# Optimization experiments

Hardware: AMD Instinct MI355X
Metric: run time of the kernel (lower is better)

Reference implementation:

```python
import jax, jax.numpy as jnp
import numpy as np

DIM = 1024
DEPTH = 3
BATCH = 8
SEQ = DIM  # module requires seq_len == dim for the residual add to broadcast


def setup_inputs() -> dict:
    key = jax.random.key(0)
    k1, k2, k3, k4 = jax.random.split(key, 4)
    x = jax.random.normal(k1, (BATCH, SEQ, DIM), dtype=jnp.float32)
    # torch.nn.Linear(dim, 3*dim): weight [3*dim, dim], bias [3*dim]
    Wqkv = jax.random.normal(k2, (3 * DIM, DIM), dtype=jnp.float32) * (1.0 / np.sqrt(DIM))
    bqkv = jax.random.normal(k3, (3 * DIM,), dtype=jnp.float32) * 0.01
    # self.w: Parameter of shape [depth, dim, dim], init randn
    w = jax.random.normal(k4, (DEPTH, DIM, DIM), dtype=jnp.float32)
    return {"x": x, "Wqkv": Wqkv, "bqkv": bqkv, "w": w}


def reference(x, Wqkv, bqkv, w):
    # qkv projection then chunk into q, k, v along last dim
    qkv = x @ Wqkv.T + bqkv                      # [B, S, 3*dim]
    q, k, v = jnp.split(qkv, 3, axis=-1)         # each [B, S, dim]
    scale = 1.0 / (q.shape[-1] ** 0.5)
    # sum over depth of (q @ w[i]) @ k^T, accumulated onto v
    # einsum contracts d (dim), e (dim), and sums over n (depth) in one pass
    scores = jnp.einsum('bsd,nde,bte->bst', q, w, k)  # [B, S, S]; requires S == dim
    return v + scores * scale
```

## Files before the change

kernel.cpp:

```cpp
#include <hip/hip_runtime.h>
#include <hip/hip_bf16.h>
#include <stdint.h>

typedef __bf16 bf16_t;
typedef __bf16 bf16x8 __attribute__((ext_vector_type(8)));
typedef __bf16 bf16x4 __attribute__((ext_vector_type(4)));
typedef float  f32x4  __attribute__((ext_vector_type(4)));

#define DIM   1024
#define BATCH 8
#define NTOK  (BATCH * DIM)
#define SCALE 0.03125f

__global__ void k_cvt(const float* __restrict__ in, bf16_t* __restrict__ out, int n4) {
    int i = blockIdx.x * blockDim.x + threadIdx.x;
    if (i < n4) {
        const float4 v = reinterpret_cast<const float4*>(in)[i];
        bf16x4 o;
        o.x = (bf16_t)v.x; o.y = (bf16_t)v.y; o.z = (bf16_t)v.z; o.w = (bf16_t)v.w;
        reinterpret_cast<bf16x4*>(out)[i] = o;
    }
}

__global__ __launch_bounds__(256)
void k_prep(const float* __restrict__ x, const float* __restrict__ Wqkv,
            const float* __restrict__ w,
            bf16_t* __restrict__ xb, bf16_t* __restrict__ wbig,
            bf16_t* __restrict__ wtb, bf16_t* __restrict__ wqt,
            float* __restrict__ bp32)
{
    __shared__ float tile[32][33];
    const int b = blockIdx.x;
    if (b < 8192) {
        const int i = b * 256 + threadIdx.x;
        const float4 v = reinterpret_cast<const float4*>(x)[i];
        bf16x4 o;
        o.x = (bf16_t)v.x; o.y = (bf16_t)v.y; o.z = (bf16_t)v.z; o.w = (bf16_t)v.w;
        reinterpret_cast<bf16x4*>(xb)[i] = o;
    } else if (b < 10240) {
        const int i = (b - 8192) * 256 + threadIdx.x;
        const float4 v = reinterpret_cast<const float4*>(Wqkv + 1048576)[i];
        bf16x4 o;
        o.x = (bf16_t)v.x; o.y = (bf16_t)v.y; o.z = (bf16_t)v.z; o.w = (bf16_t)v.w;
        reinterpret_cast<bf16x4*>(wbig + 1048576)[i] = o;
    } else if (b < 11264) {
        const int t  = b - 10240;
        const int tx = threadIdx.x & 31, ty = threadIdx.x >> 5;
        const int d0 = (t & 31) * 32, e0 = (t >> 5) * 32;
#pragma unroll
        for (int r = 0; r < 4; ++r) {
            const int d = d0 + r * 8 + ty;
            const int e = e0 + tx;
            tile[r * 8 + ty][tx] =
                w[d * 1024 + e] + w[1048576 + d * 1024 + e] + w[2097152 + d * 1024 + e];
        }
        __syncthreads();
#pragma unroll
        for (int r = 0; r < 4; ++r) {
            const int e = e0 + r * 8 + ty;
            const int d = d0 + tx;
            wtb[e * 1024 + d] = (bf16_t)tile[tx][r * 8 + ty];
        }
    } else if (b < 12288) {
        const int t  = b - 11264;
        const int tx = threadIdx.x & 31, ty = threadIdx.x >> 5;
        const int e0 = (t & 31) * 32, d0 = (t >> 5) * 32;
#pragma unroll
        for (int r = 0; r < 4; ++r)
            tile[r * 8 + ty][tx] = Wqkv[(long)(e0 + r * 8 + ty) * 1024 + d0 + tx];
        __syncthreads();
#pragma unroll
        for (int r = 0; r < 4; ++r)
            wqt[(long)(d0 + r * 8 + ty) * 1024 + e0 + tx] = (bf16_t)tile[tx][r * 8 + ty];
    } else {
        const int i = (b - 12288) * 256 + threadIdx.x;
        const f32x4 z = {0.f, 0.f, 0.f, 0.f};
        reinterpret_cast<f32x4*>(bp32)[i] = z;
    }
}

__global__ __launch_bounds__(256)
void k_mid(const float* __restrict__ bq, const bf16_t* __restrict__ wtb,
           const bf16_t* __restrict__ wqt, float* __restrict__ bqwO,
           float* __restrict__ oAt)
{
    __shared__ __align__(16) bf16_t As[128 * 32];
    __shared__ __align__(16) bf16_t Bs[128 * 32];

    const int tid  = threadIdx.x;
    const int wave = tid >> 6;
    const int lane = tid & 63;

    if (blockIdx.x < 256) {
        const int n = blockIdx.x * 4 + wave;
        const bf16_t* row = wtb + (long)n * 1024;
        float s = 0.f;
#pragma unroll
        for (int c = 0; c < 2; ++c) {
            const int d0 = (lane + c * 64) * 8;
            const bf16x8 v = *reinterpret_cast<const bf16x8*>(row + d0);
#pragma unroll
            for (int e = 0; e < 8; ++e) s += bq[d0 + e] * (float)v[e];
        }
#pragma unroll
        for (int off = 32; off; off >>= 1) s += __shfl_down(s, off);
        if (lane == 0) bqwO[n] = s;
        return;
    }

    const int s  = blockIdx.x - 256;
    const int bm = (s >> 5) * 128;
    const int bn = ((s >> 2) & 7) * 128;
    const int kb = (s & 3) * 256;
    const int wr = wave >> 1, wc = wave & 1;
    const int lhi = lane >> 4, llo = lane & 15;

    f32x4 acc[4][4];
    const f32x4 fz = {0.f, 0.f, 0.f, 0.f};
#pragma unroll
    for (int i = 0; i < 4; ++i)
#pragma unroll
        for (int j = 0; j < 4; ++j) acc[i][j] = fz;

    for (int k0 = 0; k0 < 256; k0 += 32) {
#pragma unroll
        for (int i = 0; i < 2; ++i) {
            const int c  = wave * 128 + i * 64 + lane;
            const int r  = c >> 2;
            const int cc = (c & 3) << 3;
            const long ga = (long)(bm + r) * 1024 + kb + k0 + cc;
            const long gb = (long)(bn + r) * 1024 + kb + k0 + cc;
            const int lbase = (wave * 128 + i * 64) << 3;
            __builtin_amdgcn_global_load_lds(
                (const __attribute__((address_space(1))) uint32_t*)(wtb + ga),
                (__attribute__((address_space(3))) uint32_t*)(&As[lbase]), 16, 0, 0);
            __builtin_amdgcn_global_load_lds(
                (const __attribute__((address_space(1))) uint32_t*)(wqt + gb),
                (__attribute__((address_space(3))) uint32_t*)(&Bs[lbase]), 16, 0, 0);
        }
        __syncthreads();

        bf16x8 af[4], bfr[4];
#pragma unroll
        for (int mi = 0; mi < 4; ++mi)
            af[mi] = *reinterpret_cast<const bf16x8*>(&As[(wr * 64 + mi * 16 + llo) * 32 + lhi * 8]);
#pragma unroll
        for (int ni = 0; ni < 4; ++ni)
            bfr[ni] = *reinterpret_cast<const bf16x8*>(&Bs[(wc * 64 + ni * 16 + llo) * 32 + lhi * 8]);
#pragma unroll
        for (int mi = 0; mi < 4; ++mi)
#pragma unroll
            for (int ni = 0; ni < 4; ++ni)
                acc[mi][ni] = __builtin_amdgcn_mfma_f32_16x16x32_bf16(af[mi], bfr[ni], acc[mi][ni], 0, 0, 0);
        __syncthreads();
    }

#pragma unroll
    for (int mi = 0; mi < 4; ++mi) {
        const int r0 = bm + wr * 64 + mi * 16 + lhi * 4;
#pragma unroll
        for (int ni = 0; ni < 4; ++ni) {
            const int cg = bn + wc * 64 + ni * 16 + llo;
            const f32x4 v = acc[mi][ni];
#pragma unroll
            for (int j = 0; j < 4; ++j)
                atomicAdd(&oAt[(long)(r0 + j) * 1024 + cg], v[j]);
        }
    }
}

template<int BN_, int MODE>
__global__ __launch_bounds__(512, 2)
void k_db(const bf16_t* __restrict__ A, const bf16_t* __restrict__ Bp,
          const float* __restrict__ bqw, const float* __restrict__ bqkv,
          bf16_t* __restrict__ oQW, bf16_t* __restrict__ oK, float* __restrict__ oF)
{
    constexpr int NF   = BN_ / 64;
    constexpr int LB   = BN_ / 64;
    constexpr int LPT  = 2 + LB;
    constexpr int SLOT = (128 + BN_) * 128;
    constexpr int NTT  = 16;
    __shared__ __align__(16) unsigned char slds[2 * SLOT];

    const int tid  = threadIdx.x;
    const int wave = tid >> 6, lane = tid & 63;
    const int wm = wave >> 2, wn = wave & 3;
    const int llo = lane & 15, lhi = lane >> 4;

    int bm, bn; long zz = 0;
    if (MODE == 1) {
        bm = blockIdx.x * 128; bn = blockIdx.y * BN_;
    } else {
        const int nw = ((int)blockIdx.x & 7) * 64 + ((int)blockIdx.x >> 3);
        zz = (long)(nw >> 6) << 20;
        const int r = nw & 63;
        bm = (r >> 3) * 128; bn = (r & 7) * 128;
    }

    const bf16_t* sp[LPT]; int dst[LPT];
#pragma unroll
    for (int j = 0; j < 2; ++j) {
        const int C = j * 512 + tid;
        const int r = C >> 3, u = (C & 7) ^ (r & 7);
        sp[j] = A + zz + (long)(bm + r) * 1024 + (u << 3);
        dst[j] = C << 4;
    }
#pragma unroll
    for (int j = 0; j < LB; ++j) {
        const int C = j * 512 + tid;
        const int r = C >> 3, u = (C & 7) ^ (r & 7);
        sp[2 + j] = Bp + zz + (long)(bn + r) * 1024 + (u << 3);
        dst[2 + j] = 16384 + (C << 4);
    }

    auto stage = [&](int tt) {
        unsigned char* s = &slds[(tt & 1) * SLOT];
        const long ko = (long)tt << 6;
#pragma unroll
        for (int j = 0; j < LPT; ++j)
            __builtin_amdgcn_global_load_lds(
                (const __attribute__((address_space(1))) uint32_t*)(sp[j] + ko),
                (__attribute__((address_space(3))) uint32_t*)(s + dst[j]), 16, 0, 0);
    };

    f32x4 acc[4][NF];
    const f32x4 fz = {0.f, 0.f, 0.f, 0.f};
#pragma unroll
    for (int i = 0; i < 4; ++i)
#pragma unroll
        for (int j = 0; j < NF; ++j) acc[i][j] = fz;

    stage(0);

    for (int t = 0; t < NTT; ++t) {
        if (t + 1 < NTT) {
            stage(t + 1);
            asm volatile("s_waitcnt vmcnt(%0)" :: "i"(LPT) : "memory");
        } else {
            asm volatile("s_waitcnt vmcnt(0)" ::: "memory");
        }
        __builtin_amdgcn_s_barrier();

        const unsigned char* sb = &slds[(t & 1) * SLOT];
#pragma unroll
        for (int ks = 0; ks < 2; ++ks) {
            bf16x8 af[4], bfv[NF];
#pragma unroll
            for (int mi = 0; mi < 4; ++mi) {
                const int r = wm * 64 + mi * 16 + llo;
                af[mi] = *reinterpret_cast<const bf16x8*>(
                    sb + r * 128 + ((((ks << 2) | lhi) ^ (r & 7)) << 4));
            }
#pragma unroll
            for (int ni = 0; ni < NF; ++ni) {
                const int r = wn * (NF * 16) + ni * 16 + llo;
                bfv[ni] = *reinterpret_cast<const bf16x8*>(
                    sb + 16384 + r * 128 + ((((ks << 2) | lhi) ^ (r & 7)) << 4));
            }
            __builtin_amdgcn_s_setprio(1);
#pragma unroll
            for (int mi = 0; mi < 4; ++mi)
#pragma unroll
                for (int ni = 0; ni < NF; ++ni)
                    acc[mi][ni] = __builtin_amdgcn_mfma_f32_16x16x32_bf16(
                        af[mi], bfv[ni], acc[mi][ni], 0, 0, 0);
            __builtin_amdgcn_s_setprio(0);
        }
        asm volatile("s_waitcnt lgkmcnt(0)" ::: "memory");
        __builtin_amdgcn_s_barrier();
    }

#pragma unroll
    for (int mi = 0; mi < 4; ++mi) {
        const long r0 = bm + wm * 64 + mi * 16 + lhi * 4;
#pragma unroll
        for (int ni = 0; ni < NF; ++ni) {
            const int cg = bn + wn * (NF * 16) + ni * 16 + llo;
            const f32x4 v = acc[mi][ni];
            if (MODE == 1) {
                const int sec = cg >> 10;
                const int c1  = cg & 1023;
                const float bb = (sec == 0) ? bqw[cg] : bqkv[cg];
#pragma unroll
                for (int j = 0; j < 4; ++j) {
                    const long idx = (r0 + j) * 1024 + c1;
                    const float val = v[j] + bb;
                    if (sec == 0)      oQW[idx] = (bf16_t)val;
                    else if (sec == 1) oK[idx] = (bf16_t)val;
                    else               oF[idx] = val;
                }
            } else {
#pragma unroll
                for (int j = 0; j < 4; ++j) {
                    const long idx = zz + (r0 + j) * 1024 + cg;
                    oF[idx] = oF[idx] + SCALE * v[j];
                }
            }
        }
    }
}

extern "C" void kernel_launch(void* const* d_in, const int* in_sizes, int n_in,
                              void* d_out, int out_size, void* d_ws, size_t ws_size,
                              hipStream_t stream) {
    const float* x    = (const float*)d_in[0];
    const float* Wqkv = (const float*)d_in[1];
    const float* bqkv = (const float*)d_in[2];
    const float* w    = (const float*)d_in[3];
    float* out = (float*)d_out;

    char* ws = (char*)d_ws;
    bf16_t* xb   = (bf16_t*)(ws);
    bf16_t* wbig = (bf16_t*)(ws + (16l << 20));
    float*  bqw  = (float*) (ws + (22l << 20));
    bf16_t* kb   = (bf16_t*)(ws + (22l << 20) + 65536);
    bf16_t* qwb  = (bf16_t*)(ws + (38l << 20) + 65536);
    bf16_t* wtb  = qwb;
    bf16_t* wqt  = qwb + 1048576;
    float*  bp32 = (float*)(qwb + 2097152);
    if (ws_size < (size_t)(54l << 20) + 65536) return;

    k_prep<<<13312, 256, 0, stream>>>(x, Wqkv, w, xb, wbig, wtb, wqt, bp32);

    k_mid<<<512, 256, 0, stream>>>(bqkv, wtb, wqt, bqw, bp32);

    k_cvt<<<1024, 256, 0, stream>>>(bp32, wbig, 262144);

    k_db<192, 1><<<dim3(64, 16), 512, 0, stream>>>(xb, wbig, bqw, bqkv, qwb, kb, out);

    k_db<128, 2><<<dim3(512), 512, 0, stream>>>(qwb, kb, nullptr, nullptr,
                                                nullptr, nullptr, out);
}
```

Before: 117.0 us.

## Halve k_db K-tile to 32 and raise occupancy to 4 blocks per CU

Shrinks the double-buffered LDS K-tile from 64 to 32 elements and doubles the number of K iterations, using a new swizzle that packs two 32-element rows into each 128-byte LDS line. Launch bounds go from 2 to 4 blocks per CU, meant to hide latency through more resident waves. The load schedule is reorganised, with the extra B chunk for BN=192 issued by half the waves after the barrier. In exchange there are twice as many barriers and waitcnt points per block, and register pressure is tighter under the higher occupancy bound.

```diff
diff --git a/kernel.cpp b/kernel.cpp
--- a/kernel.cpp
+++ b/kernel.cpp
@@ -169,17 +169,22 @@
     }
 }
 
+__device__ __forceinline__ int swz(int r, int c) {
+    return ((r >> 1) << 7) | (((((r & 1) << 2) | c) ^ ((r >> 1) & 7)) << 4);
+}
+#define GLOAD(SRC, DST) __builtin_amdgcn_global_load_lds( \
+    (const __attribute__((address_space(1))) uint32_t*)(SRC), \
+    (__attribute__((address_space(3))) uint32_t*)(DST), 16, 0, 0)
+
 template<int BN_, int MODE>
-__global__ __launch_bounds__(512, 2)
+__global__ __launch_bounds__(512, 4)
 void k_db(const bf16_t* __restrict__ A, const bf16_t* __restrict__ Bp,
           const float* __restrict__ bqw, const float* __restrict__ bqkv,
           bf16_t* __restrict__ oQW, bf16_t* __restrict__ oK, float* __restrict__ oF)
 {
     constexpr int NF   = BN_ / 64;
-    constexpr int LB   = BN_ / 64;
-    constexpr int LPT  = 2 + LB;
-    constexpr int SLOT = (128 + BN_) * 128;
-    constexpr int NTT  = 16;
+    constexpr int SLOT = 8192 + BN_ * 64;
+    constexpr int NTT  = 32;
     __shared__ __align__(16) unsigned char slds[2 * SLOT];
 
     const int tid  = threadIdx.x;
@@ -197,31 +202,19 @@
         bm = (r >> 3) * 128; bn = (r & 7) * 128;
     }
 
-    const bf16_t* sp[LPT]; int dst[LPT];
-#pragma unroll
-    for (int j = 0; j < 2; ++j) {
-        const int C = j * 512 + tid;
-        const int r = C >> 3, u = (C & 7) ^ (r & 7);
-        sp[j] = A + zz + (long)(bm + r) * 1024 + (u << 3);
-        dst[j] = C << 4;
-    }
-#pragma unroll
-    for (int j = 0; j < LB; ++j) {
-        const int C = j * 512 + tid;
-        const int r = C >> 3, u = (C & 7) ^ (r & 7);
-        sp[2 + j] = Bp + zz + (long)(bn + r) * 1024 + (u << 3);
-        dst[2 + j] = 16384 + (C << 4);
-    }
-
-    auto stage = [&](int tt) {
-        unsigned char* s = &slds[(tt & 1) * SLOT];
-        const long ko = (long)tt << 6;
-#pragma unroll
-        for (int j = 0; j < LPT; ++j)
-            __builtin_amdgcn_global_load_lds(
-                (const __attribute__((address_space(1))) uint32_t*)(sp[j] + ko),
-                (__attribute__((address_space(3))) uint32_t*)(s + dst[j]), 16, 0, 0);
-    };
+    const bf16_t *spA, *spB0, *spB1 = nullptr;
+    int dA, dB0, dB1 = 0;
+    {
+        const int C = tid, L = C >> 3, u = (C & 7) ^ (L & 7);
+        const int r = (L << 1) | (u >> 2), ce = (u & 3) << 3;
+        spA = A + zz + (long)(bm + r) * 1024 + ce;  dA = C << 4;
+        spB0 = Bp + zz + (long)(bn + r) * 1024 + ce; dB0 = 8192 + (C << 4);
+    }
+    if (BN_ == 192 && wave < 4) {
+        const int C = 512 + tid, L = C >> 3, u = (C & 7) ^ (L & 7);
+        const int r = (L << 1) | (u >> 2), ce = (u & 3) << 3;
+        spB1 = Bp + zz + (long)(bn + r) * 1024 + ce; dB1 = 8192 + (C << 4);
+    }
 
     f32x4 acc[4][NF];
     const f32x4 fz = {0.f, 0.f, 0.f, 0.f};
@@ -230,42 +223,47 @@
 #pragma unroll
         for (int j = 0; j < NF; ++j) acc[i][j] = fz;
 
-    stage(0);
+    {
+        unsigned char* s0 = slds;
+        GLOAD(spA, s0 + dA); GLOAD(spB0, s0 + dB0);
+        if (BN_ == 192 && wave < 4) GLOAD(spB1, s0 + dB1);
+    }
 
     for (int t = 0; t < NTT; ++t) {
         if (t + 1 < NTT) {
-            stage(t + 1);
-            asm volatile("s_waitcnt vmcnt(%0)" :: "i"(LPT) : "memory");
+            unsigned char* sn = slds + ((t + 1) & 1) * SLOT;
+            const long ko = (long)(t + 1) << 5;
+            GLOAD(spA + ko, sn + dA); GLOAD(spB0 + ko, sn + dB0);
+            asm volatile("s_waitcnt vmcnt(2)" ::: "memory");
         } else {
             asm volatile("s_waitcnt vmcnt(0)" ::: "memory");
         }
         __builtin_amdgcn_s_barrier();
-
-        const unsigned char* sb = &slds[(t & 1) * SLOT];
-#pragma unroll
-        for (int ks = 0; ks < 2; ++ks) {
-            bf16x8 af[4], bfv[NF];
-#pragma unroll
-            for (int mi = 0; mi < 4; ++mi) {
-                const int r = wm * 64 + mi * 16 + llo;
-                af[mi] = *reinterpret_cast<const bf16x8*>(
-                    sb + r * 128 + ((((ks << 2) | lhi) ^ (r & 7)) << 4));
-            }
-#pragma unroll
-            for (int ni = 0; ni < NF; ++ni) {
-                const int r = wn * (NF * 16) + ni * 16 + llo;
-                bfv[ni] = *reinterpret_cast<const bf16x8*>(
-                    sb + 16384 + r * 128 + ((((ks << 2) | lhi) ^ (r & 7)) << 4));
-            }
-            __builtin_amdgcn_s_setprio(1);
-#pragma unroll
-            for (int mi = 0; mi < 4; ++mi)
-#pragma unroll
-                for (int ni = 0; ni < NF; ++ni)
-                    acc[mi][ni] = __builtin_amdgcn_mfma_f32_16x16x32_bf16(
-                        af[mi], bfv[ni], acc[mi][ni], 0, 0, 0);
-            __builtin_amdgcn_s_setprio(0);
-        }
+        if (t + 1 < NTT && BN_ == 192 && wave < 4) {
+            unsigned char* sn = slds + ((t + 1) & 1) * SLOT;
+            GLOAD(spB1 + ((long)(t + 1) << 5), sn + dB1);
+        }
+
+        const unsigned char* sb = slds + (t & 1) * SLOT;
+        bf16x8 af[4], bfv[NF];
+#pragma unroll
+        for (int mi = 0; mi < 4; ++mi) {
+            const int r = wm * 64 + mi * 16 + llo;
+            af[mi] = *reinterpret_cast<const bf16x8*>(sb + swz(r, lhi));
+        }
+#pragma unroll
+        for (int ni = 0; ni < NF; ++ni) {
+            const int r = wn * (NF * 16) + ni * 16 + llo;
+            bfv[ni] = *reinterpret_cast<const bf16x8*>(sb + 8192 + swz(r, lhi));
+        }
+        __builtin_amdgcn_s_setprio(1);
+#pragma unroll
+        for (int mi = 0; mi < 4; ++mi)
+#pragma unroll
+            for (int ni = 0; ni < NF; ++ni)
+                acc[mi][ni] = __builtin_amdgcn_mfma_f32_16x16x32_bf16(
+                    af[mi], bfv[ni], acc[mi][ni], 0, 0, 0);
+        __builtin_amdgcn_s_setprio(0);
         asm volatile("s_waitcnt lgkmcnt(0)" ::: "memory");
         __builtin_amdgcn_s_barrier();
     }
@@ -299,6 +297,7 @@
         }
     }
 }
+#undef GLOAD
 
 extern "C" void kernel_launch(void* const* d_in, const int* in_sizes, int n_in,
                               void* d_out, int out_size, void* d_ws, size_t ws_size,
```

New measurement: 132.5 us. 13.3% more time.
